# Performance work log

Measured on AMD Instinct MI355X. Metric: run time of the kernel, lower is better.

## Reference

```python
import jax, jax.numpy as jnp
import numpy as np

N_NODES = 50000
N_EDGES = 800000
IN_DIM = 128
HID = 64
OUT_DIM = 128
N_GRAPHS = 256


def setup_inputs() -> dict:
    key = jax.random.key(0)
    ks = jax.random.split(key, 8)
    x = jax.random.normal(ks[0], (N_NODES, IN_DIM), dtype=jnp.float32)
    edge_index = jax.random.randint(ks[1], (2, N_EDGES), 0, N_NODES, dtype=jnp.int64)
    batch = jnp.sort(jax.random.randint(ks[2], (N_NODES,), 0, N_GRAPHS, dtype=jnp.int64))
    # Glorot-ish init for GCN weights, zero bias (PyG default bias=True)
    W1 = jax.random.normal(ks[3], (IN_DIM, HID), dtype=jnp.float32) / np.sqrt(IN_DIM)
    b1 = jnp.zeros((HID,), dtype=jnp.float32)
    W2 = jax.random.normal(ks[4], (HID, HID), dtype=jnp.float32) / np.sqrt(HID)
    b2 = jnp.zeros((HID,), dtype=jnp.float32)
    W3 = jax.random.normal(ks[5], (HID, OUT_DIM), dtype=jnp.float32) / np.sqrt(HID)
    b3 = jnp.zeros((OUT_DIM,), dtype=jnp.float32)
    return {"x": x, "edge_index": edge_index, "batch": batch, "num_graphs": N_GRAPHS,
            "W1": W1, "b1": b1, "W2": W2, "b2": b2, "W3": W3, "b3": b3}


def _gcn_norm(edge_index, n_nodes):
    # PyG GCNConv default: add self-loops, symmetric D^{-1/2}(A+I)D^{-1/2} norm.
    loops = jnp.arange(n_nodes, dtype=edge_index.dtype)
    src = jnp.concatenate([edge_index[0], loops])  # [E + N]
    dst = jnp.concatenate([edge_index[1], loops])
    deg = jax.ops.segment_sum(jnp.ones_like(dst, dtype=jnp.float32), dst,
                              num_segments=n_nodes)
    dinv = jnp.where(deg > 0, jax.lax.rsqrt(jnp.maximum(deg, 1.0)), 0.0)
    norm = dinv[src] * dinv[dst]  # [E + N]
    return src, dst, norm


def _gcn_conv(x, W, b, src, dst, norm, n_nodes):
    h = x @ W                                  # [N, F_out] dense GEMM
    msg = h[src] * norm[:, None]               # gather + scale  [E+N, F_out]
    agg = jax.ops.segment_sum(msg, dst, num_segments=n_nodes)
    return agg + b


def reference(x, edge_index, batch, num_graphs, W1, b1, W2, b2, W3, b3):
    n_nodes = x.shape[0]
    src, dst, norm = _gcn_norm(edge_index, n_nodes)
    h = jax.nn.gelu(_gcn_conv(x, W1, b1, src, dst, norm, n_nodes))
    h = jax.nn.gelu(_gcn_conv(h, W2, b2, src, dst, norm, n_nodes))
    h = _gcn_conv(h, W3, b3, src, dst, norm, n_nodes)
    # global_mean_pool over batch segment ids
    sums = jax.ops.segment_sum(h, batch, num_segments=num_graphs)
    counts = jax.ops.segment_sum(jnp.ones((n_nodes,), dtype=h.dtype), batch,
                                 num_segments=num_graphs)
    return sums / jnp.maximum(counts, 1.0)[:, None]
```

## Files before the change

### kernel.cpp

```cpp
#include <hip/hip_runtime.h>
#include <hip/hip_fp16.h>
#include <math.h>

#define N_NODES   50000
#define N_EDGES   800000
#define IN_DIM    128
#define HID       64
#define OUT_DIM   128
#define N_GRAPHS  256
#define MAX_DEG   64
#define PARTS     8
#define PSIZE     (N_NODES / PARTS)
#define EPB       4096
#define AGG_NPB   32
#define DEGP      32

typedef _Float16 half8 __attribute__((ext_vector_type(8)));
typedef float floatx4 __attribute__((ext_vector_type(4)));


__global__ __launch_bounds__(256) void k_build(const int* __restrict__ src,
                                               const int* __restrict__ dst,
                                               int* __restrict__ deg, int* __restrict__ col) {
    int p     = blockIdx.x & (PARTS - 1);
    int chunk = blockIdx.x >> 3;
    int e0    = chunk * EPB + threadIdx.x * 16;
    if (e0 + 16 > N_EDGES) return;
    int lo = p * PSIZE, hi = lo + PSIZE;

    int dd[16], ss[16];
    const int4* d4 = (const int4*)(dst + e0);
    const int4* s4 = (const int4*)(src + e0);
#pragma unroll
    for (int j = 0; j < 4; j++) {
        int4 q = d4[j];
        dd[4 * j + 0] = q.x; dd[4 * j + 1] = q.y;
        dd[4 * j + 2] = q.z; dd[4 * j + 3] = q.w;
    }
#pragma unroll
    for (int j = 0; j < 4; j++) {
        int4 q = s4[j];
        ss[4 * j + 0] = q.x; ss[4 * j + 1] = q.y;
        ss[4 * j + 2] = q.z; ss[4 * j + 3] = q.w;
    }

    int pos[16];
#pragma unroll
    for (int j = 0; j < 16; j++) {
        pos[j] = -1;
        if (dd[j] >= lo && dd[j] < hi) pos[j] = atomicAdd(&deg[(size_t)dd[j] * DEGP], 1);
    }
#pragma unroll
    for (int j = 0; j < 16; j++) {
        if (pos[j] >= 0 && pos[j] < MAX_DEG)
            col[(size_t)dd[j] * MAX_DEG + pos[j]] = ss[j];
    }
}

__global__ __launch_bounds__(256) void k_prep(const int* __restrict__ deg,
                                              int* __restrict__ degc,
                                              float* __restrict__ dinv,
                                              const float* __restrict__ W1, __half* __restrict__ Wt1,
                                              const float* __restrict__ W2, __half* __restrict__ Wt2) {
    int blk = blockIdx.x;
    if (blk < 196) {
        int n = blk * 256 + threadIdx.x;
        if (n < N_NODES) {
            int dg = deg[(size_t)n * DEGP];
            degc[n] = dg;
            dinv[n] = rsqrtf((float)(dg + 1));
        }
    } else if (blk < 200) {
        int idx = (blk - 196) * 256 + threadIdx.x;
        int g = idx >> 6, n = idx & 63;
#pragma unroll
        for (int i = 0; i < 8; i++)
            Wt1[idx * 8 + i] = __float2half(W1[(8 * g + i) * 64 + n]);
    } else {
        int idx = (blk - 200) * 256 + threadIdx.x;
        if (idx < 512) {
            int g = idx >> 6, n = idx & 63;
#pragma unroll
            for (int i = 0; i < 8; i++)
                Wt2[idx * 8 + i] = __float2half(W2[(8 * g + i) * 64 + n]);
        }
    }
}


__global__ __launch_bounds__(256) void k_mfma1(const float* __restrict__ A,
                                               const float* __restrict__ dinv,
                                               const __half* __restrict__ Bp,
                                               __half* __restrict__ C) {
    constexpr int K = IN_DIM, S = K / 32;
    int wv   = threadIdx.x >> 6;
    int lane = threadIdx.x & 63;
    int quad = lane >> 4, l15 = lane & 15;
    int row0 = blockIdx.x * 64 + wv * 16;
    if (row0 >= N_NODES) return;

    half8 bf[S][4];
#pragma unroll
    for (int s = 0; s < S; s++)
#pragma unroll
        for (int j = 0; j < 4; j++)
            bf[s][j] = *(const half8*)(Bp + ((size_t)((4 * s + quad) * 64 + 16 * j + l15)) * 8);

    floatx4 acc[4];
#pragma unroll
    for (int j = 0; j < 4; j++) acc[j] = 0.f;

    int arow = row0 + l15;
    float dv = dinv[arow];
#pragma unroll
    for (int s = 0; s < S; s++) {
        float4 xa = *(const float4*)(A + (size_t)arow * K + 32 * s + quad * 8);
        float4 xb = *(const float4*)(A + (size_t)arow * K + 32 * s + quad * 8 + 4);
        half8 af;
        af[0] = (_Float16)(xa.x * dv); af[1] = (_Float16)(xa.y * dv);
        af[2] = (_Float16)(xa.z * dv); af[3] = (_Float16)(xa.w * dv);
        af[4] = (_Float16)(xb.x * dv); af[5] = (_Float16)(xb.y * dv);
        af[6] = (_Float16)(xb.z * dv); af[7] = (_Float16)(xb.w * dv);
#pragma unroll
        for (int j = 0; j < 4; j++)
            acc[j] = __builtin_amdgcn_mfma_f32_16x16x32_f16(af, bf[s][j], acc[j], 0, 0, 0);
    }
#pragma unroll
    for (int j = 0; j < 4; j++)
#pragma unroll
        for (int r = 0; r < 4; r++)
            C[(size_t)(row0 + quad * 4 + r) * 64 + 16 * j + l15] = __float2half(acc[j][r]);
}


__global__ __launch_bounds__(256) void k_mfma2(const __half* __restrict__ A,
                                               const __half* __restrict__ Bp,
                                               __half* __restrict__ C) {
    constexpr int K = HID, S = K / 32;
    int wv   = threadIdx.x >> 6;
    int lane = threadIdx.x & 63;
    int quad = lane >> 4, l15 = lane & 15;
    int row0 = blockIdx.x * 64 + wv * 16;
    if (row0 >= N_NODES) return;

    half8 bf[S][4];
#pragma unroll
    for (int s = 0; s < S; s++)
#pragma unroll
        for (int j = 0; j < 4; j++)
            bf[s][j] = *(const half8*)(Bp + ((size_t)((4 * s + quad) * 64 + 16 * j + l15)) * 8);

    floatx4 acc[4];
#pragma unroll
    for (int j = 0; j < 4; j++) acc[j] = 0.f;

    int arow = row0 + l15;
#pragma unroll
    for (int s = 0; s < S; s++) {
        half8 af = *(const half8*)(A + (size_t)arow * K + 32 * s + quad * 8);
#pragma unroll
        for (int j = 0; j < 4; j++)
            acc[j] = __builtin_amdgcn_mfma_f32_16x16x32_f16(af, bf[s][j], acc[j], 0, 0, 0);
    }
#pragma unroll
    for (int j = 0; j < 4; j++)
#pragma unroll
        for (int r = 0; r < 4; r++)
            C[(size_t)(row0 + quad * 4 + r) * 64 + 16 * j + l15] = __float2half(acc[j][r]);
}


__device__ __forceinline__ void add8(float* acc, uint4 v) {
    const __half2* h = (const __half2*)&v;
#pragma unroll
    for (int j = 0; j < 4; j++) {
        acc[2 * j]     += __low2float(h[j]);
        acc[2 * j + 1] += __high2float(h[j]);
    }
}

__global__ __launch_bounds__(256) void k_agg(const __half* __restrict__ T,
                                             const int* __restrict__ col,
                                             const int* __restrict__ indeg,
                                             const float* __restrict__ dinv,
                                             const float* __restrict__ b,
                                             __half* __restrict__ OUT, int mode) {
    __shared__ int cols[AGG_NPB][MAX_DEG + 1];
    __shared__ int sdeg[AGG_NPB];
    int base = blockIdx.x * AGG_NPB;

    if (threadIdx.x < AGG_NPB) {
        int g = base + threadIdx.x;
        int dg0 = (g < N_NODES) ? indeg[g] : 0;
        sdeg[threadIdx.x] = dg0 > MAX_DEG ? MAX_DEG : dg0;
    }
    __syncthreads();

    for (int idx = threadIdx.x; idx < AGG_NPB * MAX_DEG; idx += 256) {
        int r = idx >> 6, j = idx & 63;
        if (j < sdeg[r]) cols[r][j] = col[(size_t)(base + r) * MAX_DEG + j];
    }
    __syncthreads();

    int lane = threadIdx.x & 63;
    int wv   = threadIdx.x >> 6;
    int q = lane >> 3, t = lane & 7;
    int local = wv * 8 + q;
    int d = base + local;
    if (d >= N_NODES) return;

    int dg = sdeg[local];

    float acc[8];
#pragma unroll
    for (int j = 0; j < 8; j++) acc[j] = 0.f;
    add8(acc, *(const uint4*)(T + (size_t)d * HID + t * 8));

    const int* cl = cols[local];
    int i = 0;
    for (; i + 4 <= dg; i += 4) {
        int s0 = cl[i], s1 = cl[i + 1], s2 = cl[i + 2], s3 = cl[i + 3];
        uint4 v0 = *(const uint4*)(T + (size_t)s0 * HID + t * 8);
        uint4 v1 = *(const uint4*)(T + (size_t)s1 * HID + t * 8);
        uint4 v2 = *(const uint4*)(T + (size_t)s2 * HID + t * 8);
        uint4 v3 = *(const uint4*)(T + (size_t)s3 * HID + t * 8);
        add8(acc, v0); add8(acc, v1); add8(acc, v2); add8(acc, v3);
    }
    for (; i < dg; i++) {
        int s = cl[i];
        add8(acc, *(const uint4*)(T + (size_t)s * HID + t * 8));
    }

    float dv = dinv[d];
    float o[8];
#pragma unroll
    for (int j = 0; j < 8; j++) o[j] = acc[j] * dv;
    if (mode == 0) {
#pragma unroll
        for (int j = 0; j < 8; j++) {
            float v = o[j] + b[t * 8 + j];
            float u2 = 0.7978845608028654f * (v + 0.044715f * v * v * v);
            o[j] = 0.5f * v * (1.0f + tanhf(u2)) * dv;
        }
    }
    __half2 hh[4];
#pragma unroll
    for (int j = 0; j < 4; j++) hh[j] = __floats2half2_rn(o[2 * j], o[2 * j + 1]);
    *(uint4*)(OUT + (size_t)d * HID + t * 8) = *(uint4*)hh;
}


__global__ __launch_bounds__(256) void k_pool_out(const __half* __restrict__ A,
                                                  const int* __restrict__ batch,
                                                  const float* __restrict__ W3,
                                                  const float* __restrict__ b3,
                                                  float* __restrict__ out) {
    int g = blockIdx.x;
    int lo = 0, hi = N_NODES;
    while (lo < hi) { int m = (lo + hi) >> 1; if (batch[m] < g) lo = m + 1; else hi = m; }
    int lo2 = lo, hi2 = N_NODES;
    while (lo2 < hi2) { int m = (lo2 + hi2) >> 1; if (batch[m] < g + 1) lo2 = m + 1; else hi2 = m; }
    int start = lo, end = lo2;

    int lane = threadIdx.x & 63;
    int wave = threadIdx.x >> 6;
    float acc = 0.f;
    for (int n = start + wave; n < end; n += 4)
        acc += __half2float(A[(size_t)n * HID + lane]);

    __shared__ float part[4][HID];
    __shared__ float pooled[HID];
    part[wave][lane] = acc;
    __syncthreads();
    if (threadIdx.x < HID)
        pooled[threadIdx.x] = part[0][threadIdx.x] + part[1][threadIdx.x] +
                              part[2][threadIdx.x] + part[3][threadIdx.x];
    __syncthreads();

    if (threadIdx.x < OUT_DIM) {
        float cntf = (float)(end - start);
        float inv = 1.0f / fmaxf(cntf, 1.0f);
        float s = 0.f;
#pragma unroll
        for (int k = 0; k < HID; k++) s += pooled[k] * W3[k * OUT_DIM + threadIdx.x];
        out[g * OUT_DIM + threadIdx.x] = (s + cntf * b3[threadIdx.x]) * inv;
    }
}


extern "C" void kernel_launch(void* const* d_in, const int* in_sizes, int n_in,
                              void* d_out, int out_size, void* d_ws, size_t ws_size,
                              hipStream_t stream) {
    const float* x     = (const float*)d_in[0];
    const int*   ei    = (const int*)d_in[1];
    const int*   batch = (const int*)d_in[2];
    const float* W1    = (const float*)d_in[4];
    const float* b1    = (const float*)d_in[5];
    const float* W2    = (const float*)d_in[6];
    const float* b2    = (const float*)d_in[7];
    const float* W3    = (const float*)d_in[8];
    const float* b3    = (const float*)d_in[9];
    float* out = (float*)d_out;

    const int* esrc = ei;
    const int* edst = ei + N_EDGES;

    int*    deg  = (int*)d_ws;
    int*    degc = deg + (size_t)N_NODES * DEGP;
    float*  dinv = (float*)(degc + N_NODES);
    int*    col  = (int*)(dinv + N_NODES);
    __half* t    = (__half*)(col + (size_t)N_NODES * MAX_DEG);
    __half* p    = t + (size_t)N_NODES * HID;
    __half* Wt1  = p + (size_t)N_NODES * HID;
    __half* Wt2  = Wt1 + IN_DIM * HID;

    (void)hipMemsetAsync(deg, 0, (size_t)N_NODES * DEGP * 4, stream);

    const int CHUNKS = (N_EDGES + EPB - 1) / EPB;
    k_build<<<CHUNKS * PARTS, 256, 0, stream>>>(esrc, edst, deg, col);
    k_prep<<<202, 256, 0, stream>>>(deg, degc, dinv, W1, Wt1, W2, Wt2);

    const int GB = (N_NODES + 63) / 64;
    const int AB = (N_NODES + AGG_NPB - 1) / AGG_NPB;

    k_mfma1<<<GB, 256, 0, stream>>>(x, dinv, Wt1, t);
    k_agg<<<AB, 256, 0, stream>>>(t, col, degc, dinv, b1, p, 0);
    k_mfma2<<<GB, 256, 0, stream>>>(p, Wt2, t);
    k_agg<<<AB, 256, 0, stream>>>(t, col, degc, dinv, b2, p, 0);
    k_agg<<<AB, 256, 0, stream>>>(p, col, degc, dinv, b3, t, 1);
    k_pool_out<<<N_GRAPHS, 256, 0, stream>>>(t, batch, W3, b3, out);
}
```

Measured before the change: 215.0 us.

## Sort destination nodes by degree to balance aggregation warps

Builds a degree histogram in the prep kernel, scans it, and writes a permutation that groups nodes with equal in-degree, so each aggregation block and wave handles nodes of similar degree and divergence in the neighbour loop drops. The aggregation kernel now reads node ids through this permutation. It also replaces tanhf in GELU with an exp-based formula. The cost is two extra small kernels (including a single-block scan), an extra indirection, and less locality when writing outputs and reading self rows.

```diff
diff --git a/kernel.cpp b/kernel.cpp
--- a/kernel.cpp
+++ b/kernel.cpp
@@ -14,6 +14,8 @@
 #define EPB       4096
 #define AGG_NPB   32
 #define DEGP      32
+#define NBINS     (MAX_DEG + 1)
+#define NPART     8
 
 typedef _Float16 half8 __attribute__((ext_vector_type(8)));
 typedef float floatx4 __attribute__((ext_vector_type(4)));
@@ -60,16 +62,25 @@
 __global__ __launch_bounds__(256) void k_prep(const int* __restrict__ deg,
                                               int* __restrict__ degc,
                                               float* __restrict__ dinv,
+                                              int* __restrict__ ghist,
                                               const float* __restrict__ W1, __half* __restrict__ Wt1,
                                               const float* __restrict__ W2, __half* __restrict__ Wt2) {
     int blk = blockIdx.x;
     if (blk < 196) {
+        __shared__ int lh[NBINS];
+        if (threadIdx.x < NBINS) lh[threadIdx.x] = 0;
+        __syncthreads();
         int n = blk * 256 + threadIdx.x;
         if (n < N_NODES) {
             int dg = deg[(size_t)n * DEGP];
             degc[n] = dg;
             dinv[n] = rsqrtf((float)(dg + 1));
+            int bin = dg > MAX_DEG ? MAX_DEG : dg;
+            atomicAdd(&lh[bin], 1);
         }
+        __syncthreads();
+        if (threadIdx.x < NBINS && lh[threadIdx.x])
+            atomicAdd(&ghist[threadIdx.x * NPART + (blk & (NPART - 1))], lh[threadIdx.x]);
     } else if (blk < 200) {
         int idx = (blk - 196) * 256 + threadIdx.x;
         int g = idx >> 6, n = idx & 63;
@@ -85,6 +96,34 @@
                 Wt2[idx * 8 + i] = __float2half(W2[(8 * g + i) * 64 + n]);
         }
     }
+}
+
+__global__ __launch_bounds__(1024) void k_scan(const int* __restrict__ ghist,
+                                               int* __restrict__ gcur) {
+    __shared__ int s[1024];
+    int tid = threadIdx.x;
+    const int M = NBINS * NPART;
+    s[tid] = (tid < M) ? ghist[tid] : 0;
+    __syncthreads();
+    for (int off = 1; off < 1024; off <<= 1) {
+        int v = (tid >= off) ? s[tid - off] : 0;
+        __syncthreads();
+        s[tid] += v;
+        __syncthreads();
+    }
+    if (tid < M) gcur[tid] = s[tid] - ghist[tid];
+}
+
+__global__ __launch_bounds__(256) void k_perm(const int* __restrict__ degc,
+                                              int* __restrict__ gcur,
+                                              int* __restrict__ perm) {
+    int n = blockIdx.x * 256 + threadIdx.x;
+    if (n >= N_NODES) return;
+    int dg = degc[n];
+    int bin = dg > MAX_DEG ? MAX_DEG : dg;
+    int part = (n >> 8) & (NPART - 1);
+    int pos = atomicAdd(&gcur[bin * NPART + part], 1);
+    perm[pos] = n;
 }
 
 
@@ -184,21 +223,25 @@
                                              const int* __restrict__ indeg,
                                              const float* __restrict__ dinv,
                                              const float* __restrict__ b,
+                                             const int* __restrict__ perm,
                                              __half* __restrict__ OUT, int mode) {
     __shared__ int cols[AGG_NPB][MAX_DEG + 1];
     __shared__ int sdeg[AGG_NPB];
+    __shared__ int sperm[AGG_NPB];
     int base = blockIdx.x * AGG_NPB;
 
     if (threadIdx.x < AGG_NPB) {
         int g = base + threadIdx.x;
-        int dg0 = (g < N_NODES) ? indeg[g] : 0;
+        int pn = (g < N_NODES) ? perm[g] : 0;
+        sperm[threadIdx.x] = pn;
+        int dg0 = (g < N_NODES) ? indeg[pn] : 0;
         sdeg[threadIdx.x] = dg0 > MAX_DEG ? MAX_DEG : dg0;
     }
     __syncthreads();
 
     for (int idx = threadIdx.x; idx < AGG_NPB * MAX_DEG; idx += 256) {
         int r = idx >> 6, j = idx & 63;
-        if (j < sdeg[r]) cols[r][j] = col[(size_t)(base + r) * MAX_DEG + j];
+        if (j < sdeg[r]) cols[r][j] = col[(size_t)sperm[r] * MAX_DEG + j];
     }
     __syncthreads();
 
@@ -206,9 +249,9 @@
     int wv   = threadIdx.x >> 6;
     int q = lane >> 3, t = lane & 7;
     int local = wv * 8 + q;
-    int d = base + local;
-    if (d >= N_NODES) return;
-
+    if (base + local >= N_NODES) return;
+
+    int d  = sperm[local];
     int dg = sdeg[local];
 
     float acc[8];
@@ -240,7 +283,8 @@
         for (int j = 0; j < 8; j++) {
             float v = o[j] + b[t * 8 + j];
             float u2 = 0.7978845608028654f * (v + 0.044715f * v * v * v);
-            o[j] = 0.5f * v * (1.0f + tanhf(u2)) * dv;
+            float th = 1.0f - 2.0f / (__expf(2.0f * u2) + 1.0f);
+            o[j] = 0.5f * v * (1.0f + th) * dv;
         }
     }
     __half2 hh[4];
@@ -305,28 +349,33 @@
     const int* esrc = ei;
     const int* edst = ei + N_EDGES;
 
-    int*    deg  = (int*)d_ws;
-    int*    degc = deg + (size_t)N_NODES * DEGP;
-    float*  dinv = (float*)(degc + N_NODES);
-    int*    col  = (int*)(dinv + N_NODES);
-    __half* t    = (__half*)(col + (size_t)N_NODES * MAX_DEG);
-    __half* p    = t + (size_t)N_NODES * HID;
-    __half* Wt1  = p + (size_t)N_NODES * HID;
-    __half* Wt2  = Wt1 + IN_DIM * HID;
-
-    (void)hipMemsetAsync(deg, 0, (size_t)N_NODES * DEGP * 4, stream);
+    int*    deg   = (int*)d_ws;
+    int*    ghist = deg + (size_t)N_NODES * DEGP;
+    int*    gcur  = ghist + NBINS * NPART;
+    int*    degc  = gcur + NBINS * NPART;
+    int*    perm  = degc + N_NODES;
+    float*  dinv  = (float*)(perm + N_NODES);
+    int*    col   = (int*)(dinv + N_NODES);
+    __half* t     = (__half*)(col + (size_t)N_NODES * MAX_DEG);
+    __half* p     = t + (size_t)N_NODES * HID;
+    __half* Wt1   = p + (size_t)N_NODES * HID;
+    __half* Wt2   = Wt1 + IN_DIM * HID;
+
+    (void)hipMemsetAsync(deg, 0, ((size_t)N_NODES * DEGP + 2 * NBINS * NPART) * 4, stream);
 
     const int CHUNKS = (N_EDGES + EPB - 1) / EPB;
     k_build<<<CHUNKS * PARTS, 256, 0, stream>>>(esrc, edst, deg, col);
-    k_prep<<<202, 256, 0, stream>>>(deg, degc, dinv, W1, Wt1, W2, Wt2);
+    k_prep<<<202, 256, 0, stream>>>(deg, degc, dinv, ghist, W1, Wt1, W2, Wt2);
+    k_scan<<<1, 1024, 0, stream>>>(ghist, gcur);
+    k_perm<<<196, 256, 0, stream>>>(degc, gcur, perm);
 
     const int GB = (N_NODES + 63) / 64;
     const int AB = (N_NODES + AGG_NPB - 1) / AGG_NPB;
 
     k_mfma1<<<GB, 256, 0, stream>>>(x, dinv, Wt1, t);
-    k_agg<<<AB, 256, 0, stream>>>(t, col, degc, dinv, b1, p, 0);
+    k_agg<<<AB, 256, 0, stream>>>(t, col, degc, dinv, b1, perm, p, 0);
     k_mfma2<<<GB, 256, 0, stream>>>(p, Wt2, t);
-    k_agg<<<AB, 256, 0, stream>>>(t, col, degc, dinv, b2, p, 0);
-    k_agg<<<AB, 256, 0, stream>>>(p, col, degc, dinv, b3, t, 1);
+    k_agg<<<AB, 256, 0, stream>>>(t, col, degc, dinv, b2, perm, p, 0);
+    k_agg<<<AB, 256, 0, stream>>>(p, col, degc, dinv, b3, perm, t, 1);
     k_pool_out<<<N_GRAPHS, 256, 0, stream>>>(t, batch, W3, b3, out);
 }
```

Result: slower. 328.4 us (+52.7%).
